# Kernel optimization log

Hardware: AMD Instinct MI355X
Metric: run time of the kernel (lower is better)

Reference implementation:

```python
import jax, jax.numpy as jnp
import numpy as np

N_NODES = 100000
N_EDGES = 1600000
D = 64
N_LAYERS = 3  # 1 input EdgeConv + hidden_layers(=2)
N_GRAPHS = 32
N_CLASSES = 40


def setup_inputs() -> dict:
    key = jax.random.key(0)
    ks = jax.random.split(key, 12)
    h = jax.random.normal(ks[0], (N_NODES, D), dtype=jnp.float32)
    src = jax.random.randint(ks[1], (N_EDGES,), 0, N_NODES, dtype=jnp.int32)
    dst = jax.random.randint(ks[2], (N_EDGES,), 0, N_NODES, dtype=jnp.int32)
    graph_ids = jnp.sort(jax.random.randint(ks[3], (N_NODES,), 0, N_GRAPHS, dtype=jnp.int32))
    s = 0.05
    theta_w = jax.random.normal(ks[4], (N_LAYERS, D, D), dtype=jnp.float32) * s
    theta_b = jax.random.normal(ks[5], (N_LAYERS, D), dtype=jnp.float32) * s
    phi_w = jax.random.normal(ks[6], (N_LAYERS, D, D), dtype=jnp.float32) * s
    phi_b = jax.random.normal(ks[7], (N_LAYERS, D), dtype=jnp.float32) * s
    cls_w = jax.random.normal(ks[8], (D, N_CLASSES), dtype=jnp.float32) * s
    cls_b = jax.random.normal(ks[9], (N_CLASSES,), dtype=jnp.float32) * s
    return {"h": h, "src": src, "dst": dst, "graph_ids": graph_ids,
            "theta_w": theta_w, "theta_b": theta_b, "phi_w": phi_w, "phi_b": phi_b,
            "cls_w": cls_w, "cls_b": cls_b}


def _edgeconv(h, src, dst, tw, tb, pw, pb):
    # DGL EdgeConv: h_i = max_{j in N(i)} Theta(x_j - x_i) + Phi(x_i)
    # Linearity: Theta(x_j - x_i) = (x@Theta)[j] - (x@Theta)[i]
    t = h @ tw  # [N, D]
    p = h @ pw + (tb + pb)  # fold both biases in
    msg = t[src] - t[dst] + p[dst]  # [E, D] edge messages
    agg = jax.ops.segment_max(msg, dst, num_segments=h.shape[0])
    has_in = jax.ops.segment_sum(jnp.ones((dst.shape[0],), h.dtype), dst,
                                 num_segments=h.shape[0]) > 0
    return jnp.where(has_in[:, None], agg, jnp.zeros_like(agg))  # DGL zero-fill


def reference(h, src, dst, graph_ids, theta_w, theta_b, phi_w, phi_b, cls_w, cls_b):
    # forward never applies batch_norms; dropout is identity at inference
    for l in range(N_LAYERS):
        h = _edgeconv(h, src, dst, theta_w[l], theta_b[l], phi_w[l], phi_b[l])
    # MaxPooling readout over nodes of each graph
    hg = jax.ops.segment_max(h, graph_ids, num_segments=N_GRAPHS)  # [G, D]
    return hg @ cls_w + cls_b  # [G, n_classes]
```

## Files before the change

### kernel.cpp

```cpp
#include <hip/hip_runtime.h>
#include <hip/hip_bf16.h>
#include <climits>

#define N_NODES   100000
#define N_EDGES   1600000
#define D         64
#define N_GRAPHS  32
#define N_CLASSES 40
#define N_TILES   (N_NODES / 16)
#define TPW       2
#define GEMM_WAVES ((N_TILES + TPW - 1) / TPW)
#define GEMM_BLOCKS ((GEMM_WAVES + 3) / 4)
#define POOL_NPW  32

#define BKT_SHIFT 7
#define BKT_NODES 128
#define NB        ((N_NODES + BKT_NODES - 1) / BKT_NODES)
#define CHUNK     4096
#define NCHUNK    ((N_EDGES + CHUNK - 1) / CHUNK)
#define EPT       (CHUNK / 256)

typedef _Float16 f16_t;
typedef f16_t f16x8 __attribute__((ext_vector_type(8)));
typedef f16_t f16x4 __attribute__((ext_vector_type(4)));
typedef float  f32x4  __attribute__((ext_vector_type(4)));

__device__ __forceinline__ int f2ord(float f) {
    int i = __float_as_int(f);
    return (i >= 0) ? i : (i ^ 0x7FFFFFFF);
}
__device__ __forceinline__ float ord2f(int i) {
    int j = (i >= 0) ? i : (i ^ 0x7FFFFFFF);
    return __int_as_float(j);
}

__global__ __launch_bounds__(256) void k_fill(int* __restrict__ p, long n, int v) {
    long i = (long)blockIdx.x * blockDim.x + threadIdx.x;
    long stride = (long)gridDim.x * blockDim.x;
    for (; i < n; i += stride) p[i] = v;
}

__global__ __launch_bounds__(256) void k_prep(
    const float* __restrict__ tw, const float* __restrict__ pw,
    const float* __restrict__ tb, const float* __restrict__ pb,
    f16_t* __restrict__ wcat, float* __restrict__ bcat)
{
    const int i = blockIdx.x * 256 + threadIdx.x;
    if (i < 3 * 128 * 64) {
        const int l = i >> 13;
        const int rem = i & 8191;
        const int n = rem >> 6;
        const int k = rem & 63;
        const float v = (n < D) ? tw[l * 4096 + k * D + n] : pw[l * 4096 + k * D + (n - D)];
        wcat[i] = (f16_t)v;
    }
    if (i < 3 * D) bcat[i] = tb[i] + pb[i];
}


__global__ __launch_bounds__(256) void k_bkt_hist(
    const int* __restrict__ dst, int* __restrict__ bktcnt)
{
    __shared__ int l[NB];
    for (int i = threadIdx.x; i < NB; i += 256) l[i] = 0;
    __syncthreads();
    const int base = blockIdx.x * CHUNK;
    #pragma unroll
    for (int i = 0; i < EPT; ++i) {
        const int e = base + i * 256 + threadIdx.x;
        if (e < N_EDGES) atomicAdd(&l[dst[e] >> BKT_SHIFT], 1);
    }
    __syncthreads();
    for (int i = threadIdx.x; i < NB; i += 256)
        if (l[i]) atomicAdd(&bktcnt[i], l[i]);
}

__global__ __launch_bounds__(256) void k_bkt_scan(
    const int* __restrict__ bktcnt, int* __restrict__ boff, int* __restrict__ gcur,
    int* __restrict__ rowptr)
{
    __shared__ int s[256];
    const int t = threadIdx.x;
    int v[4], sum = 0;
    #pragma unroll
    for (int i = 0; i < 4; ++i) {
        const int idx = t * 4 + i;
        v[i] = (idx < NB) ? bktcnt[idx] : 0;
        sum += v[i];
    }
    s[t] = sum;
    __syncthreads();
    #pragma unroll
    for (int off = 1; off < 256; off <<= 1) {
        int x = (t >= off) ? s[t - off] : 0;
        __syncthreads();
        s[t] += x;
        __syncthreads();
    }
    int run = s[t] - sum;
    #pragma unroll
    for (int i = 0; i < 4; ++i) {
        const int idx = t * 4 + i;
        if (idx < NB) {
            boff[idx] = run;
            gcur[idx] = run;
        }
        run += v[i];
    }
    if (t == 255) {
        boff[NB] = N_EDGES;
        rowptr[N_NODES] = N_EDGES;
    }
}

__global__ __launch_bounds__(256) void k_bkt_scatter(
    const int* __restrict__ src, const int* __restrict__ dst,
    int* __restrict__ gcur, unsigned* __restrict__ bke)
{
    __shared__ int lcnt[NB];
    __shared__ int gb[NB];
    for (int i = threadIdx.x; i < NB; i += 256) lcnt[i] = 0;
    __syncthreads();
    const int base = blockIdx.x * CHUNK;
    unsigned pk[EPT], br[EPT];
    #pragma unroll
    for (int i = 0; i < EPT; ++i) {
        const int e = base + i * 256 + threadIdx.x;
        if (e < N_EDGES) {
            const int d = dst[e];
            const int b = d >> BKT_SHIFT;
            const int r = atomicAdd(&lcnt[b], 1);
            pk[i] = ((unsigned)(d & (BKT_NODES - 1)) << 17) | (unsigned)src[e];
            br[i] = ((unsigned)b << 13) | (unsigned)r;
        } else {
            br[i] = 0xFFFFFFFFu;
        }
    }
    __syncthreads();
    for (int i = threadIdx.x; i < NB; i += 256) {
        const int c = lcnt[i];
        gb[i] = c ? atomicAdd(&gcur[i], c) : 0;
    }
    __syncthreads();
    #pragma unroll
    for (int i = 0; i < EPT; ++i) {
        if (br[i] != 0xFFFFFFFFu) {
            const int b = br[i] >> 13;
            const int r = br[i] & 8191;
            bke[gb[b] + r] = pk[i];
        }
    }
}

__global__ __launch_bounds__(256) void k_bkt_sort(
    const int* __restrict__ boff, const unsigned* __restrict__ bke,
    int* __restrict__ ebuf, int* __restrict__ rowptr)
{
    __shared__ int cnt[BKT_NODES];
    __shared__ int pfx[BKT_NODES];
    const int b = blockIdx.x;
    const int tid = threadIdx.x;
    const int beg = boff[b];
    const int end = boff[b + 1];

    if (tid < BKT_NODES) cnt[tid] = 0;
    __syncthreads();
    for (int e = beg + tid; e < end; e += 256)
        atomicAdd(&cnt[bke[e] >> 17], 1);
    __syncthreads();
    if (tid < BKT_NODES) pfx[tid] = cnt[tid];
    __syncthreads();
    #pragma unroll
    for (int off = 1; off < BKT_NODES; off <<= 1) {
        int x = 0;
        if (tid < BKT_NODES && tid >= off) x = pfx[tid - off];
        __syncthreads();
        if (tid < BKT_NODES) pfx[tid] += x;
        __syncthreads();
    }
    if (tid < BKT_NODES) {
        const int excl = pfx[tid] - cnt[tid];
        const int node = b * BKT_NODES + tid;
        if (node <= N_NODES) rowptr[node] = beg + excl;
        cnt[tid] = beg + excl;
    }
    __syncthreads();
    for (int e = beg + tid; e < end; e += 256) {
        const unsigned pk = bke[e];
        const int pos = atomicAdd(&cnt[pk >> 17], 1);
        ebuf[pos] = (int)(pk & 0x1FFFFu);
    }
}

template <bool FROM_F32>
__global__ __launch_bounds__(256) void k_gemm_mfma(
    const float* __restrict__ hf, const f16_t* __restrict__ hb,
    const f16_t* __restrict__ wcat,
    const float* __restrict__ bcat,
    f16_t* __restrict__ t, f16_t* __restrict__ q)
{
    const int lane = threadIdx.x & 63;
    const int wid  = blockIdx.x * 4 + (threadIdx.x >> 6);
    const int r16  = lane & 15;
    const int kg   = lane >> 4;
    const int koff = kg * 8;

    f16x8 bfrag[8][2];
    #pragma unroll
    for (int c = 0; c < 8; ++c)
        #pragma unroll
        for (int s = 0; s < 2; ++s)
            bfrag[c][s] = *(const f16x8*)&wcat[(c * 16 + r16) * D + s * 32 + koff];

    f32x4 bias4[4];
    #pragma unroll
    for (int c = 0; c < 4; ++c) bias4[c] = *(const f32x4*)&bcat[c * 16 + kg * 4];

    #pragma unroll
    for (int tt = 0; tt < TPW; ++tt) {
        const int tile = wid * TPW + tt;
        if (tile >= N_TILES) return;
        const long rowbase = (long)tile * 16;
        const long arow = rowbase + r16;

        f16x8 afrag[2];
        if (FROM_F32) {
            #pragma unroll
            for (int s = 0; s < 2; ++s) {
                const f32x4 v0 = *(const f32x4*)&hf[arow * D + s * 32 + koff];
                const f32x4 v1 = *(const f32x4*)&hf[arow * D + s * 32 + koff + 4];
                f16x8 a;
                a[0] = (f16_t)v0[0]; a[1] = (f16_t)v0[1];
                a[2] = (f16_t)v0[2]; a[3] = (f16_t)v0[3];
                a[4] = (f16_t)v1[0]; a[5] = (f16_t)v1[1];
                a[6] = (f16_t)v1[2]; a[7] = (f16_t)v1[3];
                afrag[s] = a;
            }
        } else {
            afrag[0] = *(const f16x8*)&hb[arow * D + koff];
            afrag[1] = *(const f16x8*)&hb[arow * D + 32 + koff];
        }

        const f32x4 zero = {0.0f, 0.0f, 0.0f, 0.0f};
        f32x4 acc[8];
        #pragma unroll
        for (int c = 0; c < 8; ++c) {
            acc[c] = __builtin_amdgcn_mfma_f32_16x16x32_f16(bfrag[c][0], afrag[0], zero, 0, 0, 0);
            acc[c] = __builtin_amdgcn_mfma_f32_16x16x32_f16(bfrag[c][1], afrag[1], acc[c], 0, 0, 0);
        }

        const long node = rowbase + r16;
        #pragma unroll
        for (int c = 0; c < 4; ++c) {
            f16x4 tv, qv;
            #pragma unroll
            for (int j = 0; j < 4; ++j) {
                const float tf = acc[c][j];
                tv[j] = (f16_t)tf;
                qv[j] = (f16_t)(acc[c + 4][j] - tf + bias4[c][j]);
            }
            *(f16x4*)&t[node * D + c * 16 + kg * 4] = tv;
            *(f16x4*)&q[node * D + c * 16 + kg * 4] = qv;
        }
    }
}

__global__ __launch_bounds__(256) void k_edge_csr(
    const int* __restrict__ rowptr, const int* __restrict__ ebuf,
    const f16_t* __restrict__ t, const f16_t* __restrict__ q,
    f16_t* __restrict__ agg)
{
    const int lane = threadIdx.x & 63;
    const int grp  = lane >> 3;
    const int g    = lane & 7;
    const int node = (blockIdx.x * 4 + (threadIdx.x >> 6)) * 8 + grp;
    const int beg = rowptr[node];
    const int end = rowptr[node + 1];
    const long nrow = (long)node * D + g * 8;

    if (end == beg) {
        f16x8 z;
        #pragma unroll
        for (int i = 0; i < 8; ++i) z[i] = (f16_t)0.0f;
        *(f16x8*)&agg[nrow] = z;
        return;
    }

    const int last = end - 1;
    f16x8 m0, m1;
    {
        int r[8];
        #pragma unroll
        for (int u = 0; u < 8; ++u) r[u] = ebuf[min(beg + u, last)];
        f16x8 v[8];
        #pragma unroll
        for (int u = 0; u < 8; ++u) v[u] = *(const f16x8*)&t[((long)r[u] << 6) + g * 8];
        m0 = __builtin_elementwise_max(__builtin_elementwise_max(v[0], v[1]),
                                       __builtin_elementwise_max(v[2], v[3]));
        m1 = __builtin_elementwise_max(__builtin_elementwise_max(v[4], v[5]),
                                       __builtin_elementwise_max(v[6], v[7]));
    }
    for (int e0 = beg + 8; e0 < end; e0 += 8) {
        int r[8];
        #pragma unroll
        for (int u = 0; u < 8; ++u) r[u] = ebuf[min(e0 + u, last)];
        f16x8 v[8];
        #pragma unroll
        for (int u = 0; u < 8; ++u) v[u] = *(const f16x8*)&t[((long)r[u] << 6) + g * 8];
        m0 = __builtin_elementwise_max(m0,
                 __builtin_elementwise_max(__builtin_elementwise_max(v[0], v[1]),
                                           __builtin_elementwise_max(v[2], v[3])));
        m1 = __builtin_elementwise_max(m1,
                 __builtin_elementwise_max(__builtin_elementwise_max(v[4], v[5]),
                                           __builtin_elementwise_max(v[6], v[7])));
    }
    const f16x8 m = __builtin_elementwise_max(m0, m1);
    const f16x8 qv = *(const f16x8*)&q[nrow];
    *(f16x8*)&agg[nrow] = m + qv;
}

__global__ __launch_bounds__(256) void k_pool(
    const f16_t* __restrict__ agg, const int* __restrict__ gid,
    int* __restrict__ hg)
{
    const int lane = threadIdx.x & 63;
    const int wave = threadIdx.x >> 6;
    const int n0 = (blockIdx.x * 4 + wave) * POOL_NPW;
    if (n0 >= N_NODES) return;
    const int nend = (n0 + POOL_NPW < N_NODES) ? n0 + POOL_NPW : N_NODES;
    int cur = gid[n0];
    float m = -INFINITY;
    for (int n = n0; n < nend; ++n) {
        const int g = gid[n];
        if (g != cur) {
            atomicMax(&hg[cur * D + lane], f2ord(m));
            cur = g;
            m = -INFINITY;
        }
        m = fmaxf(m, (float)agg[(long)n * D + lane]);
    }
    atomicMax(&hg[cur * D + lane], f2ord(m));
}

__global__ __launch_bounds__(256) void k_cls(
    const int* __restrict__ hg, const float* __restrict__ w,
    const float* __restrict__ b, float* __restrict__ out)
{
    __shared__ float s_h[N_GRAPHS * D];
    __shared__ float s_w[D * N_CLASSES];
    __shared__ float s_b[N_CLASSES];
    for (int i = threadIdx.x; i < N_GRAPHS * D; i += 256) s_h[i] = ord2f(hg[i]);
    for (int i = threadIdx.x; i < D * N_CLASSES; i += 256) s_w[i] = w[i];
    if (threadIdx.x < N_CLASSES) s_b[threadIdx.x] = b[threadIdx.x];
    __syncthreads();
    for (int o = threadIdx.x; o < N_GRAPHS * N_CLASSES; o += 256) {
        const int g = o / N_CLASSES;
        const int c = o % N_CLASSES;
        float acc = s_b[c];
        #pragma unroll
        for (int k = 0; k < D; ++k)
            acc = fmaf(s_h[g * D + k], s_w[k * N_CLASSES + c], acc);
        out[o] = acc;
    }
}

extern "C" void kernel_launch(void* const* d_in, const int* in_sizes, int n_in,
                              void* d_out, int out_size, void* d_ws, size_t ws_size,
                              hipStream_t stream) {
    const float* h       = (const float*)d_in[0];
    const int*   src     = (const int*)d_in[1];
    const int*   dst     = (const int*)d_in[2];
    const int*   gid     = (const int*)d_in[3];
    const float* theta_w = (const float*)d_in[4];
    const float* theta_b = (const float*)d_in[5];
    const float* phi_w   = (const float*)d_in[6];
    const float* phi_b   = (const float*)d_in[7];
    const float* cls_w   = (const float*)d_in[8];
    const float* cls_b   = (const float*)d_in[9];
    float* out = (float*)d_out;

    const size_t NF = (size_t)N_NODES * D;
    char* p = (char*)d_ws;
    f16_t* t     = (f16_t*)p;   p += NF * 2;
    f16_t* q     = (f16_t*)p;   p += NF * 2;
    f16_t* agg   = (f16_t*)p;   p += NF * 2;
    f16_t* wcat  = (f16_t*)p;   p += 3 * 128 * D * 2;
    float*  bcat = (float*)p;   p += 3 * D * 4;
    unsigned* bke = (unsigned*)p; p += (size_t)N_EDGES * 4;
    int* ebuf    = (int*)p;     p += (size_t)N_EDGES * 4;
    int* rowptr  = (int*)p;     p += (N_NODES + 1) * 4;
    int* bktcnt  = (int*)p;     p += NB * 4;
    int* boff    = (int*)p;     p += (NB + 1) * 4;
    int* gcur    = (int*)p;     p += NB * 4;
    int* hg      = (int*)p;     p += N_GRAPHS * D * 4;
    const size_t need = (size_t)(p - (char*)d_ws);
    if (ws_size < need) {
        hipMemsetAsync(d_out, 0, (size_t)out_size * sizeof(float), stream);
        return;
    }

    const int EDGE_GRID = N_NODES / 32;
    const int POOL_GRID = (N_NODES + POOL_NPW * 4 - 1) / (POOL_NPW * 4);

    k_prep<<<96, 256, 0, stream>>>(theta_w, phi_w, theta_b, phi_b, wcat, bcat);

    k_fill<<<4, 256, 0, stream>>>(bktcnt, NB, 0);
    k_bkt_hist<<<NCHUNK, 256, 0, stream>>>(dst, bktcnt);
    k_bkt_scan<<<1, 256, 0, stream>>>(bktcnt, boff, gcur, rowptr);
    k_bkt_scatter<<<NCHUNK, 256, 0, stream>>>(src, dst, gcur, bke);
    k_bkt_sort<<<NB, 256, 0, stream>>>(boff, bke, ebuf, rowptr);

    k_gemm_mfma<true><<<GEMM_BLOCKS, 256, 0, stream>>>(h, nullptr, wcat, bcat, t, q);
    k_edge_csr<<<EDGE_GRID, 256, 0, stream>>>(rowptr, ebuf, t, q, agg);

    k_gemm_mfma<false><<<GEMM_BLOCKS, 256, 0, stream>>>(
        nullptr, agg, wcat + 128 * D, bcat + D, t, q);
    k_edge_csr<<<EDGE_GRID, 256, 0, stream>>>(rowptr, ebuf, t, q, agg);

    k_gemm_mfma<false><<<GEMM_BLOCKS, 256, 0, stream>>>(
        nullptr, agg, wcat + 2 * 128 * D, bcat + 2 * D, t, q);
    k_edge_csr<<<EDGE_GRID, 256, 0, stream>>>(rowptr, ebuf, t, q, agg);

    k_fill<<<8, 256, 0, stream>>>(hg, (long)(N_GRAPHS * D), INT_MIN);
    k_pool<<<POOL_GRID, 256, 0, stream>>>(agg, gid, hg);
    k_cls<<<1, 256, 0, stream>>>(hg, cls_w, cls_b, out);
}
```

Baseline: 245.4 us.

## Fuse fills into prep, merge gemm0 with histogram, fuse pooling into last edge pass

Moves the two fill kernels into k_prep. Co-launches the first GEMM and the bucket histogram in one grid so they run side by side. Folds graph max-pooling into the final edge aggregation pass, using a wave shuffle reduction followed by atomics. This removes several launches and a separate pass over agg, at the cost of more atomics in the last edge kernel and a heavier mixed-role kernel.

```diff
diff --git a/kernel.cpp b/kernel.cpp
--- a/kernel.cpp
+++ b/kernel.cpp
@@ -11,7 +11,6 @@
 #define TPW       2
 #define GEMM_WAVES ((N_TILES + TPW - 1) / TPW)
 #define GEMM_BLOCKS ((GEMM_WAVES + 3) / 4)
-#define POOL_NPW  32
 
 #define BKT_SHIFT 7
 #define BKT_NODES 128
@@ -34,16 +33,19 @@
     return __int_as_float(j);
 }
 
-__global__ __launch_bounds__(256) void k_fill(int* __restrict__ p, long n, int v) {
-    long i = (long)blockIdx.x * blockDim.x + threadIdx.x;
-    long stride = (long)gridDim.x * blockDim.x;
-    for (; i < n; i += stride) p[i] = v;
+__device__ __forceinline__ f16x8 shflxor8(f16x8 v, int mask) {
+    union { f16x8 h; int i[4]; } u;
+    u.h = v;
+    #pragma unroll
+    for (int d = 0; d < 4; ++d) u.i[d] = __shfl_xor(u.i[d], mask, 64);
+    return u.h;
 }
 
 __global__ __launch_bounds__(256) void k_prep(
     const float* __restrict__ tw, const float* __restrict__ pw,
     const float* __restrict__ tb, const float* __restrict__ pb,
-    f16_t* __restrict__ wcat, float* __restrict__ bcat)
+    f16_t* __restrict__ wcat, float* __restrict__ bcat,
+    int* __restrict__ bktcnt, int* __restrict__ hg)
 {
     const int i = blockIdx.x * 256 + threadIdx.x;
     if (i < 3 * 128 * 64) {
@@ -55,25 +57,93 @@
         wcat[i] = (f16_t)v;
     }
     if (i < 3 * D) bcat[i] = tb[i] + pb[i];
-}
-
-
-__global__ __launch_bounds__(256) void k_bkt_hist(
+    if (i < NB) bktcnt[i] = 0;
+    if (i < N_GRAPHS * D) hg[i] = INT_MIN;
+}
+
+__global__ __launch_bounds__(256) void k_gemm0_hist(
+    const float* __restrict__ hf,
+    const f16_t* __restrict__ wcat, const float* __restrict__ bcat,
+    f16_t* __restrict__ t, f16_t* __restrict__ q,
     const int* __restrict__ dst, int* __restrict__ bktcnt)
 {
     __shared__ int l[NB];
-    for (int i = threadIdx.x; i < NB; i += 256) l[i] = 0;
-    __syncthreads();
-    const int base = blockIdx.x * CHUNK;
-    #pragma unroll
-    for (int i = 0; i < EPT; ++i) {
-        const int e = base + i * 256 + threadIdx.x;
-        if (e < N_EDGES) atomicAdd(&l[dst[e] >> BKT_SHIFT], 1);
-    }
-    __syncthreads();
-    for (int i = threadIdx.x; i < NB; i += 256)
-        if (l[i]) atomicAdd(&bktcnt[i], l[i]);
-}
+    if (blockIdx.x >= GEMM_BLOCKS) {
+        const int bb = blockIdx.x - GEMM_BLOCKS;
+        for (int i = threadIdx.x; i < NB; i += 256) l[i] = 0;
+        __syncthreads();
+        const int base = bb * CHUNK;
+        #pragma unroll
+        for (int i = 0; i < EPT; ++i) {
+            const int e = base + i * 256 + threadIdx.x;
+            if (e < N_EDGES) atomicAdd(&l[dst[e] >> BKT_SHIFT], 1);
+        }
+        __syncthreads();
+        for (int i = threadIdx.x; i < NB; i += 256)
+            if (l[i]) atomicAdd(&bktcnt[i], l[i]);
+        return;
+    }
+    const int lane = threadIdx.x & 63;
+    const int wid  = blockIdx.x * 4 + (threadIdx.x >> 6);
+    const int r16  = lane & 15;
+    const int kg   = lane >> 4;
+    const int koff = kg * 8;
+
+    f16x8 bfrag[8][2];
+    #pragma unroll
+    for (int c = 0; c < 8; ++c)
+        #pragma unroll
+        for (int s = 0; s < 2; ++s)
+            bfrag[c][s] = *(const f16x8*)&wcat[(c * 16 + r16) * D + s * 32 + koff];
+
+    f32x4 bias4[4];
+    #pragma unroll
+    for (int c = 0; c < 4; ++c) bias4[c] = *(const f32x4*)&bcat[c * 16 + kg * 4];
+
+    #pragma unroll
+    for (int tt = 0; tt < TPW; ++tt) {
+        const int tile = wid * TPW + tt;
+        if (tile >= N_TILES) return;
+        const long rowbase = (long)tile * 16;
+        const long arow = rowbase + r16;
+
+        f16x8 afrag[2];
+        #pragma unroll
+        for (int s = 0; s < 2; ++s) {
+            const f32x4 v0 = *(const f32x4*)&hf[arow * D + s * 32 + koff];
+            const f32x4 v1 = *(const f32x4*)&hf[arow * D + s * 32 + koff + 4];
+            f16x8 a;
+            a[0] = (f16_t)v0[0]; a[1] = (f16_t)v0[1];
+            a[2] = (f16_t)v0[2]; a[3] = (f16_t)v0[3];
+            a[4] = (f16_t)v1[0]; a[5] = (f16_t)v1[1];
+            a[6] = (f16_t)v1[2]; a[7] = (f16_t)v1[3];
+            afrag[s] = a;
+        }
+
+        const f32x4 zero = {0.0f, 0.0f, 0.0f, 0.0f};
+        f32x4 acc[8];
+        #pragma unroll
+        for (int c = 0; c < 8; ++c) {
+            acc[c] = __builtin_amdgcn_mfma_f32_16x16x32_f16(bfrag[c][0], afrag[0], zero, 0, 0, 0);
+            acc[c] = __builtin_amdgcn_mfma_f32_16x16x32_f16(bfrag[c][1], afrag[1], acc[c], 0, 0, 0);
+        }
+
+        const long node = rowbase + r16;
+        #pragma unroll
+        for (int c = 0; c < 4; ++c) {
+            f16x4 tv, qv;
+            #pragma unroll
+            for (int j = 0; j < 4; ++j) {
+                const float tf = acc[c][j];
+                tv[j] = (f16_t)tf;
+                qv[j] = (f16_t)(acc[c + 4][j] - tf + bias4[c][j]);
+            }
+            *(f16x4*)&t[node * D + c * 16 + kg * 4] = tv;
+            *(f16x4*)&q[node * D + c * 16 + kg * 4] = qv;
+        }
+    }
+}
+
 
 __global__ __launch_bounds__(256) void k_bkt_scan(
     const int* __restrict__ bktcnt, int* __restrict__ boff, int* __restrict__ gcur,
@@ -192,9 +262,8 @@
     }
 }
 
-template <bool FROM_F32>
 __global__ __launch_bounds__(256) void k_gemm_mfma(
-    const float* __restrict__ hf, const f16_t* __restrict__ hb,
+    const f16_t* __restrict__ hb,
     const f16_t* __restrict__ wcat,
     const float* __restrict__ bcat,
     f16_t* __restrict__ t, f16_t* __restrict__ q)
@@ -224,22 +293,8 @@
         const long arow = rowbase + r16;
 
         f16x8 afrag[2];
-        if (FROM_F32) {
-            #pragma unroll
-            for (int s = 0; s < 2; ++s) {
-                const f32x4 v0 = *(const f32x4*)&hf[arow * D + s * 32 + koff];
-                const f32x4 v1 = *(const f32x4*)&hf[arow * D + s * 32 + koff + 4];
-                f16x8 a;
-                a[0] = (f16_t)v0[0]; a[1] = (f16_t)v0[1];
-                a[2] = (f16_t)v0[2]; a[3] = (f16_t)v0[3];
-                a[4] = (f16_t)v1[0]; a[5] = (f16_t)v1[1];
-                a[6] = (f16_t)v1[2]; a[7] = (f16_t)v1[3];
-                afrag[s] = a;
-            }
-        } else {
-            afrag[0] = *(const f16x8*)&hb[arow * D + koff];
-            afrag[1] = *(const f16x8*)&hb[arow * D + 32 + koff];
-        }
+        afrag[0] = *(const f16x8*)&hb[arow * D + koff];
+        afrag[1] = *(const f16x8*)&hb[arow * D + 32 + koff];
 
         const f32x4 zero = {0.0f, 0.0f, 0.0f, 0.0f};
         f32x4 acc[8];
@@ -265,10 +320,11 @@
     }
 }
 
+template <bool POOL>
 __global__ __launch_bounds__(256) void k_edge_csr(
     const int* __restrict__ rowptr, const int* __restrict__ ebuf,
     const f16_t* __restrict__ t, const f16_t* __restrict__ q,
-    f16_t* __restrict__ agg)
+    f16_t* __restrict__ agg, const int* __restrict__ gid, int* __restrict__ hg)
 {
     const int lane = threadIdx.x & 63;
     const int grp  = lane >> 3;
@@ -278,68 +334,65 @@
     const int end = rowptr[node + 1];
     const long nrow = (long)node * D + g * 8;
 
+    f16x8 o;
     if (end == beg) {
-        f16x8 z;
-        #pragma unroll
-        for (int i = 0; i < 8; ++i) z[i] = (f16_t)0.0f;
-        *(f16x8*)&agg[nrow] = z;
-        return;
-    }
-
-    const int last = end - 1;
-    f16x8 m0, m1;
-    {
-        int r[8];
-        #pragma unroll
-        for (int u = 0; u < 8; ++u) r[u] = ebuf[min(beg + u, last)];
-        f16x8 v[8];
-        #pragma unroll
-        for (int u = 0; u < 8; ++u) v[u] = *(const f16x8*)&t[((long)r[u] << 6) + g * 8];
-        m0 = __builtin_elementwise_max(__builtin_elementwise_max(v[0], v[1]),
-                                       __builtin_elementwise_max(v[2], v[3]));
-        m1 = __builtin_elementwise_max(__builtin_elementwise_max(v[4], v[5]),
-                                       __builtin_elementwise_max(v[6], v[7]));
-    }
-    for (int e0 = beg + 8; e0 < end; e0 += 8) {
-        int r[8];
-        #pragma unroll
-        for (int u = 0; u < 8; ++u) r[u] = ebuf[min(e0 + u, last)];
-        f16x8 v[8];
-        #pragma unroll
-        for (int u = 0; u < 8; ++u) v[u] = *(const f16x8*)&t[((long)r[u] << 6) + g * 8];
-        m0 = __builtin_elementwise_max(m0,
-                 __builtin_elementwise_max(__builtin_elementwise_max(v[0], v[1]),
-                                           __builtin_elementwise_max(v[2], v[3])));
-        m1 = __builtin_elementwise_max(m1,
-                 __builtin_elementwise_max(__builtin_elementwise_max(v[4], v[5]),
-                                           __builtin_elementwise_max(v[6], v[7])));
-    }
-    const f16x8 m = __builtin_elementwise_max(m0, m1);
-    const f16x8 qv = *(const f16x8*)&q[nrow];
-    *(f16x8*)&agg[nrow] = m + qv;
-}
-
-__global__ __launch_bounds__(256) void k_pool(
-    const f16_t* __restrict__ agg, const int* __restrict__ gid,
-    int* __restrict__ hg)
-{
-    const int lane = threadIdx.x & 63;
-    const int wave = threadIdx.x >> 6;
-    const int n0 = (blockIdx.x * 4 + wave) * POOL_NPW;
-    if (n0 >= N_NODES) return;
-    const int nend = (n0 + POOL_NPW < N_NODES) ? n0 + POOL_NPW : N_NODES;
-    int cur = gid[n0];
-    float m = -INFINITY;
-    for (int n = n0; n < nend; ++n) {
-        const int g = gid[n];
-        if (g != cur) {
-            atomicMax(&hg[cur * D + lane], f2ord(m));
-            cur = g;
-            m = -INFINITY;
-        }
-        m = fmaxf(m, (float)agg[(long)n * D + lane]);
-    }
-    atomicMax(&hg[cur * D + lane], f2ord(m));
+        #pragma unroll
+        for (int i = 0; i < 8; ++i) o[i] = (f16_t)0.0f;
+    } else {
+        const f16x8 qv = *(const f16x8*)&q[nrow];
+        const int last = end - 1;
+        f16x8 m0, m1;
+        {
+            int r[8];
+            #pragma unroll
+            for (int u = 0; u < 8; ++u) r[u] = ebuf[min(beg + u, last)];
+            f16x8 v[8];
+            #pragma unroll
+            for (int u = 0; u < 8; ++u) v[u] = *(const f16x8*)&t[((long)r[u] << 6) + g * 8];
+            m0 = __builtin_elementwise_max(__builtin_elementwise_max(v[0], v[1]),
+                                           __builtin_elementwise_max(v[2], v[3]));
+            m1 = __builtin_elementwise_max(__builtin_elementwise_max(v[4], v[5]),
+                                           __builtin_elementwise_max(v[6], v[7]));
+        }
+        for (int e0 = beg + 8; e0 < end; e0 += 8) {
+            int r[8];
+            #pragma unroll
+            for (int u = 0; u < 8; ++u) r[u] = ebuf[min(e0 + u, last)];
+            f16x8 v[8];
+            #pragma unroll
+            for (int u = 0; u < 8; ++u) v[u] = *(const f16x8*)&t[((long)r[u] << 6) + g * 8];
+            m0 = __builtin_elementwise_max(m0,
+                     __builtin_elementwise_max(__builtin_elementwise_max(v[0], v[1]),
+                                               __builtin_elementwise_max(v[2], v[3])));
+            m1 = __builtin_elementwise_max(m1,
+                     __builtin_elementwise_max(__builtin_elementwise_max(v[4], v[5]),
+                                               __builtin_elementwise_max(v[6], v[7])));
+        }
+        o = __builtin_elementwise_max(m0, m1) + qv;
+    }
+
+    if (!POOL) {
+        *(f16x8*)&agg[nrow] = o;
+    } else {
+        const int g0 = gid[node];
+        const int gf = __shfl(g0, 0);
+        const int gl = __shfl(g0, 63);
+        if (gf == gl) {
+            f16x8 m = o;
+            m = __builtin_elementwise_max(m, shflxor8(m, 8));
+            m = __builtin_elementwise_max(m, shflxor8(m, 16));
+            m = __builtin_elementwise_max(m, shflxor8(m, 32));
+            if (grp == 0) {
+                #pragma unroll
+                for (int i = 0; i < 8; ++i)
+                    atomicMax(&hg[gf * D + g * 8 + i], f2ord((float)m[i]));
+            }
+        } else {
+            #pragma unroll
+            for (int i = 0; i < 8; ++i)
+                atomicMax(&hg[g0 * D + g * 8 + i], f2ord((float)o[i]));
+        }
+    }
 }
 
 __global__ __launch_bounds__(256) void k_cls(
@@ -400,28 +453,22 @@
     }
 
     const int EDGE_GRID = N_NODES / 32;
-    const int POOL_GRID = (N_NODES + POOL_NPW * 4 - 1) / (POOL_NPW * 4);
-
-    k_prep<<<96, 256, 0, stream>>>(theta_w, phi_w, theta_b, phi_b, wcat, bcat);
-
-    k_fill<<<4, 256, 0, stream>>>(bktcnt, NB, 0);
-    k_bkt_hist<<<NCHUNK, 256, 0, stream>>>(dst, bktcnt);
+
+    k_prep<<<96, 256, 0, stream>>>(theta_w, phi_w, theta_b, phi_b, wcat, bcat, bktcnt, hg);
+
+    k_gemm0_hist<<<GEMM_BLOCKS + NCHUNK, 256, 0, stream>>>(h, wcat, bcat, t, q, dst, bktcnt);
+
     k_bkt_scan<<<1, 256, 0, stream>>>(bktcnt, boff, gcur, rowptr);
     k_bkt_scatter<<<NCHUNK, 256, 0, stream>>>(src, dst, gcur, bke);
     k_bkt_sort<<<NB, 256, 0, stream>>>(boff, bke, ebuf, rowptr);
 
-    k_gemm_mfma<true><<<GEMM_BLOCKS, 256, 0, stream>>>(h, nullptr, wcat, bcat, t, q);
-    k_edge_csr<<<EDGE_GRID, 256, 0, stream>>>(rowptr, ebuf, t, q, agg);
-
-    k_gemm_mfma<false><<<GEMM_BLOCKS, 256, 0, stream>>>(
-        nullptr, agg, wcat + 128 * D, bcat + D, t, q);
-    k_edge_csr<<<EDGE_GRID, 256, 0, stream>>>(rowptr, ebuf, t, q, agg);
-
-    k_gemm_mfma<false><<<GEMM_BLOCKS, 256, 0, stream>>>(
-        nullptr, agg, wcat + 2 * 128 * D, bcat + 2 * D, t, q);
-    k_edge_csr<<<EDGE_GRID, 256, 0, stream>>>(rowptr, ebuf, t, q, agg);
-
-    k_fill<<<8, 256, 0, stream>>>(hg, (long)(N_GRAPHS * D), INT_MIN);
-    k_pool<<<POOL_GRID, 256, 0, stream>>>(agg, gid, hg);
+    k_edge_csr<false><<<EDGE_GRID, 256, 0, stream>>>(rowptr, ebuf, t, q, agg, gid, hg);
+
+    k_gemm_mfma<<<GEMM_BLOCKS, 256, 0, stream>>>(agg, wcat + 128 * D, bcat + D, t, q);
+    k_edge_csr<false><<<EDGE_GRID, 256, 0, stream>>>(rowptr, ebuf, t, q, agg, gid, hg);
+
+    k_gemm_mfma<<<GEMM_BLOCKS, 256, 0, stream>>>(agg, wcat + 2 * 128 * D, bcat + 2 * D, t, q);
+    k_edge_csr<true><<<EDGE_GRID, 256, 0, stream>>>(rowptr, ebuf, t, q, agg, gid, hg);
+
     k_cls<<<1, 256, 0, stream>>>(hg, cls_w, cls_b, out);
 }
```

Result: slower. 377.5 us (+53.9%).
